# Kernel tuning notes

Measured on AMD Instinct MI355X. Metric: run time of the kernel, lower is better.

Reference implementation:

```python
import jax, jax.numpy as jnp
import numpy as np


def setup_inputs() -> dict:
    key = jax.random.key(0)
    k1, k2 = jax.random.split(key)
    B, T, D = 32, 512, 384
    x = jax.random.normal(k1, (B, T, D), dtype=jnp.float32)
    duration = jax.random.randint(k2, (B, T), 0, 8, dtype=jnp.int64)
    max_len = 2048
    return {"x": x, "duration": duration, "max_len": max_len}


def reference(x, duration, max_len):
    # x: [B, T, D] phoneme-level features; duration: [B, T] int frame counts.
    # Frame j of utterance b copies phoneme i where cumsum(dur)[i-1] <= j < cumsum(dur)[i].
    B, T, D = x.shape
    cum = jnp.cumsum(duration, axis=1)                      # [B, T] exclusive upper bounds
    pos = jnp.arange(max_len)                               # [L]
    # searchsorted(side='right') maps frame index -> source phoneme index
    idx = jax.vmap(lambda c: jnp.searchsorted(c, pos, side="right"))(cum)  # [B, L]
    mel_len = cum[:, -1]                                    # [B] true expanded lengths
    valid = pos[None, :] < mel_len[:, None]                 # [B, L] pad mask
    idx_c = jnp.clip(idx, 0, T - 1)
    out = jnp.take_along_axis(x, idx_c[:, :, None], axis=1) # [B, L, D] gather
    out = jnp.where(valid[:, :, None], out, jnp.zeros((), dtype=x.dtype))
    return out, mel_len
```

## Files before the change

### kernel.cpp

```cpp
#include <hip/hip_runtime.h>


#define T_IN   512
#define D_DIM  384
#define D4     (D_DIM / 4)
#define MAXLEN 2048
#define B_SZ   32
#define ROWS_PER_BLOCK 16

typedef float f32x4 __attribute__((ext_vector_type(4)));

__global__ __launch_bounds__(256) void lr_fused_kernel(const float* __restrict__ x,
                                                       const int* __restrict__ dur,
                                                       float* __restrict__ out,
                                                       float* __restrict__ mel_out) {
    __shared__ int scum[T_IN];
    __shared__ int sp[256];
    __shared__ int sidx[ROWS_PER_BLOCK];
    const int b = blockIdx.y;
    const int tid = threadIdx.x;

    int2 d2 = ((const int2*)(dur + b * T_IN))[tid];
    const int pair = d2.x + d2.y;
    sp[tid] = pair;
    __syncthreads();
    #pragma unroll
    for (int off = 1; off < 256; off <<= 1) {
        int v = sp[tid];
        int add = (tid >= off) ? sp[tid - off] : 0;
        __syncthreads();
        sp[tid] = v + add;
        __syncthreads();
    }
    const int excl = sp[tid] - pair;
    scum[2 * tid]     = excl + d2.x;
    scum[2 * tid + 1] = excl + d2.x + d2.y;
    __syncthreads();

    const int mel = scum[T_IN - 1];
    if (blockIdx.x == 0 && tid == 0) mel_out[b] = (float)mel;

    if (tid < ROWS_PER_BLOCK) {
        const int p = blockIdx.x * ROWS_PER_BLOCK + tid;
        int lo = 0, hi = T_IN;
        while (lo < hi) {
            int mid = (lo + hi) >> 1;
            if (scum[mid] <= p) lo = mid + 1; else hi = mid;
        }
        if (lo > T_IN - 1) lo = T_IN - 1;
        sidx[tid] = (p < mel) ? lo : -1;
    }
    __syncthreads();

    const f32x4* __restrict__ x4 = (const f32x4*)x;
    f32x4* __restrict__ out4 =
        (f32x4*)out + ((size_t)b * MAXLEN + (size_t)blockIdx.x * ROWS_PER_BLOCK) * D4;
    #pragma unroll
    for (int i = 0; i < 6; ++i) {
        int flat = i * 256 + tid;
        int row = flat / D4;
        int chunk = flat - row * D4;
        int idx = sidx[row];
        f32x4 v = (f32x4)(0.f);
        if (idx >= 0)
            v = x4[((size_t)b * T_IN + idx) * D4 + chunk];
        __builtin_nontemporal_store(v, &out4[flat]);
    }
}

extern "C" void kernel_launch(void* const* d_in, const int* in_sizes, int n_in,
                              void* d_out, int out_size, void* d_ws, size_t ws_size,
                              hipStream_t stream) {
    const float* x = (const float*)d_in[0];
    const int* dur = (const int*)d_in[1];

    float* out = (float*)d_out;
    float* mel_out = out + (size_t)B_SZ * MAXLEN * D_DIM;

    dim3 grid(MAXLEN / ROWS_PER_BLOCK, B_SZ);
    lr_fused_kernel<<<grid, 256, 0, stream>>>(x, dur, out, mel_out);
}
```

Before: 24.65 us.

## Use wave-shuffle prefix scan and process four row groups per block

Swaps the shared-memory Hillis-Steele scan, which needed many block barriers, for a 64-lane shuffle scan plus a small cross-wave fixup. Each block now copies 64 output rows instead of 16, so the per-block duration scan is spread over four times as much copy work and the grid is four times smaller. The trade-off is fewer blocks in flight, which may reduce memory-level parallelism.

```diff
diff --git a/kernel.cpp b/kernel.cpp
--- a/kernel.cpp
+++ b/kernel.cpp
@@ -6,7 +6,9 @@
 #define D4     (D_DIM / 4)
 #define MAXLEN 2048
 #define B_SZ   32
-#define ROWS_PER_BLOCK 16
+#define ROWS_PER_GROUP 16
+#define GROUPS_PER_BLOCK 4
+#define ROWS_PER_BLOCK (ROWS_PER_GROUP * GROUPS_PER_BLOCK)
 
 typedef float f32x4 __attribute__((ext_vector_type(4)));
 
@@ -15,24 +17,28 @@
                                                        float* __restrict__ out,
                                                        float* __restrict__ mel_out) {
     __shared__ int scum[T_IN];
-    __shared__ int sp[256];
+    __shared__ int wsum[4];
     __shared__ int sidx[ROWS_PER_BLOCK];
     const int b = blockIdx.y;
     const int tid = threadIdx.x;
+    const int lane = tid & 63;
+    const int wave = tid >> 6;
 
     int2 d2 = ((const int2*)(dur + b * T_IN))[tid];
     const int pair = d2.x + d2.y;
-    sp[tid] = pair;
+    int v = pair;
+    #pragma unroll
+    for (int off = 1; off < 64; off <<= 1) {
+        int u = __shfl_up(v, off, 64);
+        if (lane >= off) v += u;
+    }
+    if (lane == 63) wsum[wave] = v;
     __syncthreads();
+    int wprefix = 0;
     #pragma unroll
-    for (int off = 1; off < 256; off <<= 1) {
-        int v = sp[tid];
-        int add = (tid >= off) ? sp[tid - off] : 0;
-        __syncthreads();
-        sp[tid] = v + add;
-        __syncthreads();
-    }
-    const int excl = sp[tid] - pair;
+    for (int w = 0; w < 4; ++w) wprefix += (w < wave) ? wsum[w] : 0;
+    v += wprefix;
+    const int excl = v - pair;
     scum[2 * tid]     = excl + d2.x;
     scum[2 * tid + 1] = excl + d2.x + d2.y;
     __syncthreads();
@@ -52,19 +58,22 @@
     }
     __syncthreads();
 
-    const f32x4* __restrict__ x4 = (const f32x4*)x;
+    const f32x4* __restrict__ x4 = (const f32x4*)x + (size_t)b * T_IN * D4;
     f32x4* __restrict__ out4 =
         (f32x4*)out + ((size_t)b * MAXLEN + (size_t)blockIdx.x * ROWS_PER_BLOCK) * D4;
-    #pragma unroll
-    for (int i = 0; i < 6; ++i) {
-        int flat = i * 256 + tid;
-        int row = flat / D4;
-        int chunk = flat - row * D4;
-        int idx = sidx[row];
-        f32x4 v = (f32x4)(0.f);
-        if (idx >= 0)
-            v = x4[((size_t)b * T_IN + idx) * D4 + chunk];
-        __builtin_nontemporal_store(v, &out4[flat]);
+    for (int g = 0; g < GROUPS_PER_BLOCK; ++g) {
+        f32x4* __restrict__ o4 = out4 + (size_t)g * ROWS_PER_GROUP * D4;
+        #pragma unroll
+        for (int i = 0; i < 6; ++i) {
+            int flat = i * 256 + tid;
+            int row = flat / D4;
+            int chunk = flat - row * D4;
+            int idx = sidx[g * ROWS_PER_GROUP + row];
+            f32x4 val = (f32x4)(0.f);
+            if (idx >= 0)
+                val = x4[(size_t)idx * D4 + chunk];
+            __builtin_nontemporal_store(val, &o4[flat]);
+        }
     }
 }
 
```

Result: slower. 25.76 us (+4.5%).
